# Performance work log

Hardware: AMD Instinct MI355X
Metric: run time of the kernel (lower is better)

## Reference

```python
import jax, jax.numpy as jnp
import numpy as np

NEG_INF = -1.0e9


def setup_inputs() -> dict:
    key = jax.random.key(0)
    ks = jax.random.split(key, 8)
    B, H, S, D = 8, 8, 1024, 64
    return {
        "gv_feat": jax.random.normal(ks[0], (B, D), dtype=jnp.float32),
        "query2": jax.random.normal(ks[1], (B, H, S, D), dtype=jnp.float32),
        "key": jax.random.normal(ks[2], (B, H, S, D), dtype=jnp.float32),
        "att_mask": jax.random.randint(ks[3], (B, S), 0, 2, dtype=jnp.int32),
        "value1": jax.random.normal(ks[4], (B, H, S, D), dtype=jnp.float32),
        "value2": jax.random.normal(ks[5], (B, H, S, D), dtype=jnp.float32),
        "W_ch": jax.random.normal(ks[6], (D, D), dtype=jnp.float32) * (1.0 / np.sqrt(D)),
        "b_ch": jnp.zeros((D,), dtype=jnp.float32),
    }


def reference(gv_feat, query2, key, att_mask, value1, value2, W_ch, b_ch):
    # query2/key/value1/value2: [B, H, S, D]; att_mask: [B, S]
    D = query2.shape[-1]
    scaling = D ** (-0.5)
    # spatial attention: masked scaled QK^T softmax
    scores = jnp.einsum("bhqd,bhkd->bhqk", query2, key) * scaling  # [B,H,S,S]
    mask = att_mask[:, None, None, :]  # [B,1,1,S]
    scores = jnp.where(mask == 0, NEG_INF, scores)
    alpha_spatial = jax.nn.softmax(scores, axis=-1)
    attn2 = jnp.einsum("bhqk,bhkd->bhqd", alpha_spatial, value2)  # [B,H,S,D]
    # channel attention: sigmoid-gated linear over elementwise value1*key
    att_map_channel = value1 * key  # [B,H,S,D]
    alpha_channel = jax.nn.sigmoid(
        jnp.einsum("bhsd,ed->bhse", att_map_channel, W_ch) + b_ch
    )
    attn2 = alpha_channel * attn2
    return (gv_feat, attn2)
```

## Files before the change

kernel.cpp:

```cpp
#include <hip/hip_runtime.h>
#include <hip/hip_bf16.h>

typedef __attribute__((ext_vector_type(4)))  float f32x4;
typedef __attribute__((ext_vector_type(16))) float f32x16;
typedef __attribute__((ext_vector_type(8)))  short bf16x8;
typedef __attribute__((ext_vector_type(4)))  unsigned u32x4;
typedef __attribute__((ext_vector_type(2)))  unsigned u32x2;

#define NEG_INF_F (-1000000000.0f)

__device__ inline unsigned pkbf(float a, float b) {
    union { __hip_bfloat16 h; unsigned short u; } x, y;
    x.h = __float2bfloat16(a);
    y.h = __float2bfloat16(b);
    return (unsigned)x.u | ((unsigned)y.u << 16);
}

__global__ __launch_bounds__(512) void aoa_attn_kernel(
    const float* __restrict__ gv,
    const float* __restrict__ q2,
    const float* __restrict__ keyp,
    const int*   __restrict__ maskp,
    const float* __restrict__ v1,
    const float* __restrict__ v2,
    const float* __restrict__ W,
    const float* __restrict__ bch,
    float* __restrict__ out)
{
    constexpr int S = 1024, D = 64;
    const int bh  = blockIdx.x;
    const int qt  = blockIdx.y;
    const int b   = bh >> 3;
    const int tid = threadIdx.x;
    const int wid = tid >> 6;
    const int lane = tid & 63;
    const int l31 = lane & 31;
    const int h   = lane >> 5;

    float* out_attn = out + 512;
    if (bh == 0 && qt == 0) out[tid] = gv[tid];

    __shared__ float maskf[S];
    __shared__ short Klds[2][64][72];
    __shared__ short Vt[2][64][72];
    __shared__ float Lw[8][32];

    for (int i = tid; i < S; i += 512)
        maskf[i] = maskp[b * S + i] ? 0.0f : NEG_INF_F;

    const size_t base = (size_t)bh * S * D;
    const float* Qp  = q2   + base;
    const float* Kp  = keyp + base;
    const float* V1p = v1   + base;
    const float* V2p = v2   + base;

    const int q0   = qt * 256 + wid * 32;
    const int qrow = q0 + l31;

    bf16x8 bq[4];
    #pragma unroll
    for (int ds = 0; ds < 4; ++ds) {
        const f32x4* p = (const f32x4*)(Qp + (size_t)qrow * D + ds * 16 + h * 8);
        f32x4 x0 = p[0], x1 = p[1];
        u32x4 u = (u32x4){pkbf(x0[0], x0[1]), pkbf(x0[2], x0[3]),
                          pkbf(x1[0], x1[1]), pkbf(x1[2], x1[3])};
        bq[ds] = *(bf16x8*)&u;
    }

    f32x16 acc_o[2];
    #pragma unroll
    for (int dh = 0; dh < 2; ++dh)
        #pragma unroll
        for (int r = 0; r < 16; ++r) acc_o[dh][r] = 0.0f;

    float m_run = -1e30f, l_run = 0.0f;
    const float SC = 0.125f * 1.4426950408889634f;

    const int kk   = tid >> 3;
    const int d0   = (tid & 7) << 3;
    const int dcol = tid & 63;
    const int kr0  = (tid >> 6) << 3;

    f32x4 kA, kB;
    float vv[8];
    {
        const f32x4* src = (const f32x4*)(Kp + (size_t)kk * D + d0);
        kA = src[0]; kB = src[1];
        #pragma unroll
        for (int i = 0; i < 8; ++i) vv[i] = V2p[(size_t)(kr0 + i) * D + dcol];
    }
    *(u32x4*)&Klds[0][kk][d0] = (u32x4){pkbf(kA[0], kA[1]), pkbf(kA[2], kA[3]),
                                        pkbf(kB[0], kB[1]), pkbf(kB[2], kB[3])};
    *(u32x4*)&Vt[0][dcol][kr0] = (u32x4){pkbf(vv[0], vv[1]), pkbf(vv[2], vv[3]),
                                         pkbf(vv[4], vv[5]), pkbf(vv[6], vv[7])};
    int cur = 0;

    for (int t = 0; t < 16; ++t) {
        const int kt = t * 64;
        __syncthreads();

        if (t < 15) {
            const f32x4* src = (const f32x4*)(Kp + (size_t)(kt + 64 + kk) * D + d0);
            kA = src[0]; kB = src[1];
            #pragma unroll
            for (int i = 0; i < 8; ++i) vv[i] = V2p[(size_t)(kt + 64 + kr0 + i) * D + dcol];
        }

        f32x16 accs[2];
        __builtin_amdgcn_s_setprio(1);
        #pragma unroll
        for (int sub = 0; sub < 2; ++sub) {
            f32x16 a;
            #pragma unroll
            for (int r = 0; r < 16; ++r) a[r] = 0.0f;
            #pragma unroll
            for (int ds = 0; ds < 4; ++ds) {
                bf16x8 ak = *(const bf16x8*)&Klds[cur][sub * 32 + l31][ds * 16 + h * 8];
                a = __builtin_amdgcn_mfma_f32_32x32x16_bf16(ak, bq[ds], a, 0, 0, 0);
            }
            accs[sub] = a;
        }
        __builtin_amdgcn_s_setprio(0);

        float s[32];
        float tmax = -1e30f;
        #pragma unroll
        for (int sub = 0; sub < 2; ++sub)
            #pragma unroll
            for (int g = 0; g < 4; ++g) {
                f32x4 mk = *(const f32x4*)&maskf[kt + sub * 32 + g * 8 + h * 4];
                #pragma unroll
                for (int j = 0; j < 4; ++j) {
                    float val = fmaf(accs[sub][g * 4 + j], SC, mk[j]);
                    s[sub * 16 + g * 4 + j] = val;
                    tmax = fmaxf(tmax, val);
                }
            }
        tmax = fmaxf(tmax, __shfl_xor(tmax, 32));

        if (__any(tmax > m_run + 8.0f)) {
            float mnew = fmaxf(m_run, tmax);
            float r = __builtin_amdgcn_exp2f(m_run - mnew);
            l_run *= r;
            #pragma unroll
            for (int dh = 0; dh < 2; ++dh)
                #pragma unroll
                for (int r2 = 0; r2 < 16; ++r2) acc_o[dh][r2] *= r;
            m_run = mnew;
        }

        float psum = 0.0f;
        unsigned w[16];
        #pragma unroll
        for (int i = 0; i < 16; ++i) {
            float p0 = __builtin_amdgcn_exp2f(s[2 * i]     - m_run);
            float p1 = __builtin_amdgcn_exp2f(s[2 * i + 1] - m_run);
            psum += p0 + p1;
            w[i] = pkbf(p0, p1);
        }
        psum += __shfl_xor(psum, 32);
        l_run += psum;

        __builtin_amdgcn_s_setprio(1);
        #pragma unroll
        for (int sub = 0; sub < 2; ++sub) {
            #pragma unroll
            for (int t2 = 0; t2 < 2; ++t2) {
                const int wb = sub * 8 + t2 * 4;
                u32x2 r0 = __builtin_amdgcn_permlane32_swap(w[wb + 0], w[wb + 2], false, false);
                u32x2 r1 = __builtin_amdgcn_permlane32_swap(w[wb + 1], w[wb + 3], false, false);
                u32x4 ua = (u32x4){r0[0], r1[0], r0[1], r1[1]};
                bf16x8 pa = *(bf16x8*)&ua;
                #pragma unroll
                for (int dh = 0; dh < 2; ++dh) {
                    bf16x8 bv = *(const bf16x8*)&Vt[cur][dh * 32 + l31][sub * 32 + t2 * 16 + h * 8];
                    acc_o[dh] = __builtin_amdgcn_mfma_f32_32x32x16_bf16(pa, bv, acc_o[dh], 0, 0, 0);
                }
            }
        }
        __builtin_amdgcn_s_setprio(0);

        if (t < 15) {
            *(u32x4*)&Klds[cur ^ 1][kk][d0] = (u32x4){pkbf(kA[0], kA[1]), pkbf(kA[2], kA[3]),
                                                      pkbf(kB[0], kB[1]), pkbf(kB[2], kB[3])};
            *(u32x4*)&Vt[cur ^ 1][dcol][kr0] = (u32x4){pkbf(vv[0], vv[1]), pkbf(vv[2], vv[3]),
                                                       pkbf(vv[4], vv[5]), pkbf(vv[6], vv[7])};
        }
        cur ^= 1;
    }

    f32x16 acc_g[2];
    #pragma unroll
    for (int eh = 0; eh < 2; ++eh)
        #pragma unroll
        for (int r = 0; r < 16; ++r) acc_g[eh][r] = 0.0f;

    bf16x8 bam[4];
    #pragma unroll
    for (int ds = 0; ds < 4; ++ds) {
        const f32x4* p1 = (const f32x4*)(V1p + (size_t)qrow * D + ds * 16 + h * 8);
        const f32x4* pk = (const f32x4*)(Kp  + (size_t)qrow * D + ds * 16 + h * 8);
        f32x4 a0 = p1[0], a1 = p1[1], c0 = pk[0], c1 = pk[1];
        u32x4 u = (u32x4){pkbf(a0[0] * c0[0], a0[1] * c0[1]), pkbf(a0[2] * c0[2], a0[3] * c0[3]),
                          pkbf(a1[0] * c1[0], a1[1] * c1[1]), pkbf(a1[2] * c1[2], a1[3] * c1[3])};
        bam[ds] = *(bf16x8*)&u;
    }
    #pragma unroll
    for (int eh = 0; eh < 2; ++eh) {
        #pragma unroll
        for (int ds = 0; ds < 4; ++ds) {
            const f32x4* pw = (const f32x4*)(W + (size_t)(eh * 32 + l31) * D + ds * 16 + h * 8);
            f32x4 x0 = pw[0], x1 = pw[1];
            u32x4 u = (u32x4){pkbf(x0[0], x0[1]), pkbf(x0[2], x0[3]),
                              pkbf(x1[0], x1[1]), pkbf(x1[2], x1[3])};
            bf16x8 bw = *(bf16x8*)&u;
            acc_g[eh] = __builtin_amdgcn_mfma_f32_32x32x16_bf16(bam[ds], bw, acc_g[eh], 0, 0, 0);
        }
    }

    Lw[wid][l31] = 1.0f / l_run;
    __builtin_amdgcn_wave_barrier();
    const float bv0 = bch[l31], bv1 = bch[32 + l31];
    #pragma unroll
    for (int dh = 0; dh < 2; ++dh) {
        const float bc = dh ? bv1 : bv0;
        #pragma unroll
        for (int r = 0; r < 16; ++r) {
            const int ql = (r & 3) + 8 * (r >> 2) + 4 * h;
            float invl = Lw[wid][ql];
            float o = acc_o[dh][r] * invl;
            float z = acc_g[dh][r] + bc;
            float gate = 1.0f / (1.0f + __expf(-z));
            out_attn[base + (size_t)(q0 + ql) * D + dh * 32 + l31] = o * gate;
        }
    }
}

extern "C" void kernel_launch(void* const* d_in, const int* in_sizes, int n_in,
                              void* d_out, int out_size, void* d_ws, size_t ws_size,
                              hipStream_t stream) {
    const float* gv   = (const float*)d_in[0];
    const float* q2   = (const float*)d_in[1];
    const float* keyp = (const float*)d_in[2];
    const int*   mask = (const int*)  d_in[3];
    const float* v1   = (const float*)d_in[4];
    const float* v2   = (const float*)d_in[5];
    const float* W    = (const float*)d_in[6];
    const float* bch  = (const float*)d_in[7];
    float* out = (float*)d_out;

    dim3 grid(64, 4);
    aoa_attn_kernel<<<grid, 512, 0, stream>>>(gv, q2, keyp, mask, v1, v2, W, bch, out);
}
```

Baseline: 48.15 us.

## Split 64-key tile into two 32-key softmax halves to interleave MFMA and VALU

Each 64-key tile's online softmax is now processed as two independent 32-key halves. Each half does its own max, rescale and exp, and then its own PV MFMAs. Both QK accumulators are still computed up front, so the second half's exp work can overlap with the first half's PV MFMAs. The s_setprio hints are removed. The cost is up to twice as many max checks, cross-lane shuffles and rescale branches per tile, with fewer live score registers.

```diff
diff --git a/kernel.cpp b/kernel.cpp
--- a/kernel.cpp
+++ b/kernel.cpp
@@ -106,79 +106,124 @@
             for (int i = 0; i < 8; ++i) vv[i] = V2p[(size_t)(kt + 64 + kr0 + i) * D + dcol];
         }
 
-        f32x16 accs[2];
-        __builtin_amdgcn_s_setprio(1);
-        #pragma unroll
-        for (int sub = 0; sub < 2; ++sub) {
-            f32x16 a;
-            #pragma unroll
-            for (int r = 0; r < 16; ++r) a[r] = 0.0f;
-            #pragma unroll
-            for (int ds = 0; ds < 4; ++ds) {
-                bf16x8 ak = *(const bf16x8*)&Klds[cur][sub * 32 + l31][ds * 16 + h * 8];
-                a = __builtin_amdgcn_mfma_f32_32x32x16_bf16(ak, bq[ds], a, 0, 0, 0);
-            }
-            accs[sub] = a;
-        }
-        __builtin_amdgcn_s_setprio(0);
-
-        float s[32];
-        float tmax = -1e30f;
-        #pragma unroll
-        for (int sub = 0; sub < 2; ++sub)
+        f32x16 a0;
+        #pragma unroll
+        for (int r = 0; r < 16; ++r) a0[r] = 0.0f;
+        #pragma unroll
+        for (int ds = 0; ds < 4; ++ds) {
+            bf16x8 ak = *(const bf16x8*)&Klds[cur][l31][ds * 16 + h * 8];
+            a0 = __builtin_amdgcn_mfma_f32_32x32x16_bf16(ak, bq[ds], a0, 0, 0, 0);
+        }
+        f32x16 a1;
+        #pragma unroll
+        for (int r = 0; r < 16; ++r) a1[r] = 0.0f;
+        #pragma unroll
+        for (int ds = 0; ds < 4; ++ds) {
+            bf16x8 ak = *(const bf16x8*)&Klds[cur][32 + l31][ds * 16 + h * 8];
+            a1 = __builtin_amdgcn_mfma_f32_32x32x16_bf16(ak, bq[ds], a1, 0, 0, 0);
+        }
+
+        unsigned w0[8];
+        {
+            float s[16];
+            float tmax = -1e30f;
             #pragma unroll
             for (int g = 0; g < 4; ++g) {
-                f32x4 mk = *(const f32x4*)&maskf[kt + sub * 32 + g * 8 + h * 4];
+                f32x4 mk = *(const f32x4*)&maskf[kt + g * 8 + h * 4];
                 #pragma unroll
                 for (int j = 0; j < 4; ++j) {
-                    float val = fmaf(accs[sub][g * 4 + j], SC, mk[j]);
-                    s[sub * 16 + g * 4 + j] = val;
+                    float val = fmaf(a0[g * 4 + j], SC, mk[j]);
+                    s[g * 4 + j] = val;
                     tmax = fmaxf(tmax, val);
                 }
             }
-        tmax = fmaxf(tmax, __shfl_xor(tmax, 32));
-
-        if (__any(tmax > m_run + 8.0f)) {
-            float mnew = fmaxf(m_run, tmax);
-            float r = __builtin_amdgcn_exp2f(m_run - mnew);
-            l_run *= r;
-            #pragma unroll
-            for (int dh = 0; dh < 2; ++dh)
-                #pragma unroll
-                for (int r2 = 0; r2 < 16; ++r2) acc_o[dh][r2] *= r;
-            m_run = mnew;
-        }
-
-        float psum = 0.0f;
-        unsigned w[16];
-        #pragma unroll
-        for (int i = 0; i < 16; ++i) {
-            float p0 = __builtin_amdgcn_exp2f(s[2 * i]     - m_run);
-            float p1 = __builtin_amdgcn_exp2f(s[2 * i + 1] - m_run);
-            psum += p0 + p1;
-            w[i] = pkbf(p0, p1);
-        }
-        psum += __shfl_xor(psum, 32);
-        l_run += psum;
-
-        __builtin_amdgcn_s_setprio(1);
-        #pragma unroll
-        for (int sub = 0; sub < 2; ++sub) {
-            #pragma unroll
-            for (int t2 = 0; t2 < 2; ++t2) {
-                const int wb = sub * 8 + t2 * 4;
-                u32x2 r0 = __builtin_amdgcn_permlane32_swap(w[wb + 0], w[wb + 2], false, false);
-                u32x2 r1 = __builtin_amdgcn_permlane32_swap(w[wb + 1], w[wb + 3], false, false);
-                u32x4 ua = (u32x4){r0[0], r1[0], r0[1], r1[1]};
-                bf16x8 pa = *(bf16x8*)&ua;
-                #pragma unroll
-                for (int dh = 0; dh < 2; ++dh) {
-                    bf16x8 bv = *(const bf16x8*)&Vt[cur][dh * 32 + l31][sub * 32 + t2 * 16 + h * 8];
-                    acc_o[dh] = __builtin_amdgcn_mfma_f32_32x32x16_bf16(pa, bv, acc_o[dh], 0, 0, 0);
+            tmax = fmaxf(tmax, __shfl_xor(tmax, 32));
+            if (__any(tmax > m_run + 8.0f)) {
+                float mnew = fmaxf(m_run, tmax);
+                float r = __builtin_amdgcn_exp2f(m_run - mnew);
+                l_run *= r;
+                #pragma unroll
+                for (int dh = 0; dh < 2; ++dh)
+                    #pragma unroll
+                    for (int r2 = 0; r2 < 16; ++r2) acc_o[dh][r2] *= r;
+                m_run = mnew;
+            }
+            float ps0 = 0.f, ps1 = 0.f;
+            #pragma unroll
+            for (int i = 0; i < 8; ++i) {
+                float p0 = __builtin_amdgcn_exp2f(s[2 * i]     - m_run);
+                float p1 = __builtin_amdgcn_exp2f(s[2 * i + 1] - m_run);
+                ps0 += p0; ps1 += p1;
+                w0[i] = pkbf(p0, p1);
+            }
+            float psum = ps0 + ps1;
+            psum += __shfl_xor(psum, 32);
+            l_run += psum;
+        }
+
+        #pragma unroll
+        for (int t2 = 0; t2 < 2; ++t2) {
+            u32x2 r0 = __builtin_amdgcn_permlane32_swap(w0[t2 * 4 + 0], w0[t2 * 4 + 2], false, false);
+            u32x2 r1 = __builtin_amdgcn_permlane32_swap(w0[t2 * 4 + 1], w0[t2 * 4 + 3], false, false);
+            u32x4 ua = (u32x4){r0[0], r1[0], r0[1], r1[1]};
+            bf16x8 pa = *(bf16x8*)&ua;
+            #pragma unroll
+            for (int dh = 0; dh < 2; ++dh) {
+                bf16x8 bv = *(const bf16x8*)&Vt[cur][dh * 32 + l31][t2 * 16 + h * 8];
+                acc_o[dh] = __builtin_amdgcn_mfma_f32_32x32x16_bf16(pa, bv, acc_o[dh], 0, 0, 0);
+            }
+        }
+
+        unsigned w1[8];
+        {
+            float s[16];
+            float tmax = -1e30f;
+            #pragma unroll
+            for (int g = 0; g < 4; ++g) {
+                f32x4 mk = *(const f32x4*)&maskf[kt + 32 + g * 8 + h * 4];
+                #pragma unroll
+                for (int j = 0; j < 4; ++j) {
+                    float val = fmaf(a1[g * 4 + j], SC, mk[j]);
+                    s[g * 4 + j] = val;
+                    tmax = fmaxf(tmax, val);
                 }
             }
-        }
-        __builtin_amdgcn_s_setprio(0);
+            tmax = fmaxf(tmax, __shfl_xor(tmax, 32));
+            if (__any(tmax > m_run + 8.0f)) {
+                float mnew = fmaxf(m_run, tmax);
+                float r = __builtin_amdgcn_exp2f(m_run - mnew);
+                l_run *= r;
+                #pragma unroll
+                for (int dh = 0; dh < 2; ++dh)
+                    #pragma unroll
+                    for (int r2 = 0; r2 < 16; ++r2) acc_o[dh][r2] *= r;
+                m_run = mnew;
+            }
+            float ps0 = 0.f, ps1 = 0.f;
+            #pragma unroll
+            for (int i = 0; i < 8; ++i) {
+                float p0 = __builtin_amdgcn_exp2f(s[2 * i]     - m_run);
+                float p1 = __builtin_amdgcn_exp2f(s[2 * i + 1] - m_run);
+                ps0 += p0; ps1 += p1;
+                w1[i] = pkbf(p0, p1);
+            }
+            float psum = ps0 + ps1;
+            psum += __shfl_xor(psum, 32);
+            l_run += psum;
+        }
+
+        #pragma unroll
+        for (int t2 = 0; t2 < 2; ++t2) {
+            u32x2 r0 = __builtin_amdgcn_permlane32_swap(w1[t2 * 4 + 0], w1[t2 * 4 + 2], false, false);
+            u32x2 r1 = __builtin_amdgcn_permlane32_swap(w1[t2 * 4 + 1], w1[t2 * 4 + 3], false, false);
+            u32x4 ua = (u32x4){r0[0], r1[0], r0[1], r1[1]};
+            bf16x8 pa = *(bf16x8*)&ua;
+            #pragma unroll
+            for (int dh = 0; dh < 2; ++dh) {
+                bf16x8 bv = *(const bf16x8*)&Vt[cur][dh * 32 + l31][32 + t2 * 16 + h * 8];
+                acc_o[dh] = __builtin_amdgcn_mfma_f32_32x32x16_bf16(pa, bv, acc_o[dh], 0, 0, 0);
+            }
+        }
 
         if (t < 15) {
             *(u32x4*)&Klds[cur ^ 1][kk][d0] = (u32x4){pkbf(kA[0], kA[1]), pkbf(kA[2], kA[3]),
```

Result: faster. 46.93 us (-2.5%).
